# Kernel tuning notes

Measured on AMD Instinct MI355X. Metric: run time of the kernel, lower is better.

The kernel has to match this reference:

```python
import jax, jax.numpy as jnp
import numpy as np

EPS = 1e-7
LABEL_SMOOTHING = 0.1

def label2onehot(labels, pad_value):
    # labels: [B,T] int -> multi-hot [B, pad_value] with pad column dropped and index 0 zeroed
    oh = jax.nn.one_hot(labels, pad_value + 1, dtype=jnp.float32)  # [B,T,P+1]
    oh = oh.max(axis=1)[:, :-1]                                    # [B,P]
    return oh.at[:, 0].set(0.0)

def mask_from_eos(ids, eos_value):
    # mult_before=False variant: mask[:,0]=1, mask[:,t]=prod_{j=1..t}(ids[:,j]!=eos)
    ne = (ids != eos_value).astype(jnp.float32)
    ne = ne.at[:, 0].set(1.0)
    return jnp.cumprod(ne, axis=1)

def bce(p, t):
    p = jnp.clip(p, EPS, 1.0 - EPS)
    return -(t * jnp.log(p) + (1.0 - t) * jnp.log1p(-p))

def setup_inputs():
    key = jax.random.key(0)
    k1, k2, k3 = jax.random.split(key, 3)
    B, T, P = 4096, 20, 1488  # batch, max ingredients, ingredient vocab (= pad_value)
    return {
        "ingr_logits": jax.random.normal(k1, (B, T, P), dtype=jnp.float32),
        "target_ingrs": jax.random.randint(k2, (B, T), 0, P + 1, dtype=jnp.int32),
        "ingr_ids": jax.random.randint(k3, (B, T), 0, P + 1, dtype=jnp.int32),
        "pad_value": P,
    }

def reference(ingr_logits, target_ingrs, ingr_ids, pad_value):
    probs = jax.nn.softmax(ingr_logits, axis=-1)            # [B,T,P]
    eos = probs[:, :, 0]                                    # [B,T]

    t_oh = label2onehot(target_ingrs, pad_value)            # [B,P]
    denom = jnp.float32(t_oh.shape[-1])
    t_oh_smooth = jnp.where(t_oh == 0, LABEL_SMOOTHING / denom, 1.0 - LABEL_SMOOTHING)

    target_eos = ((target_ingrs == 0) ^ (target_ingrs == pad_value)).astype(jnp.float32)
    eos_pos = (target_ingrs == 0).astype(jnp.float32)
    eos_head = ((target_ingrs != pad_value) & (target_ingrs != 0)).astype(jnp.float32)

    mask = mask_from_eos(target_ingrs, 0)                   # [B,T]
    ingr_probs = (probs * mask[:, :, None]).max(axis=1)     # [B,P] permutation-invariant max
    ingr_ids_m = jnp.where(mask == 0, pad_value, ingr_ids)

    ingr_loss = bce(ingr_probs, t_oh_smooth).mean()

    card_penalty = (jnp.abs((ingr_probs * t_oh).sum(axis=1))
                    - t_oh.sum(axis=1)
                    + jnp.abs((ingr_probs * (1.0 - t_oh)).sum(axis=1)))

    eos_l = bce(eos, target_eos)                            # [B,T]
    mult = 0.5
    eos_loss = (mult * (eos_l * eos_pos).sum(axis=1) / (eos_pos.sum(axis=1) + 1e-6)
                + mult * (eos_l * eos_head).sum(axis=1) / (eos_head.sum(axis=1) + 1e-6))

    pred_oh = label2onehot(ingr_ids_m, pad_value)           # [B,P]
    num = (pred_oh * t_oh).sum(axis=1)
    den = (pred_oh + t_oh - pred_oh * t_oh).sum(axis=1) + 1e-6
    iou = 1.0 - num / den                                   # softIoU loss per sample

    return (ingr_loss, card_penalty, eos_loss, iou)
```

## Files before the change

kernel.cpp:

```cpp
#include <hip/hip_runtime.h>
#include <math.h>

#define BATCH 4096
#define TSEQ  20
#define PDIM  1488
#define PADV  1488
#define NV    372
#define NT    384
#define NW    6
#define EPSF  1e-7f

__device__ __forceinline__ float bce_f(float p, float t) {
    p = fminf(fmaxf(p, EPSF), 1.0f - EPSF);
    return -(t * logf(p) + (1.0f - t) * log1pf(-p));
}

__global__ __launch_bounds__(NT) void icm_main_kernel(
    const float* __restrict__ logits,
    const int*   __restrict__ target,
    const int*   __restrict__ ids,
    float*       __restrict__ out,
    float*       __restrict__ ws)
{
    const int b    = blockIdx.x;
    const int tid  = threadIdx.x;
    const int lane = tid & 63;
    const int wid  = tid >> 6;

    __shared__ int   s_tgt[TSEQ];
    __shared__ int   s_ids[TSEQ];
    __shared__ float s_mask[TSEQ];
    __shared__ float s_maxbuf[NW];
    __shared__ float s_sumbuf[NW];
    __shared__ unsigned char s_toh[PDIM];
    __shared__ unsigned char s_pred[PDIM];

    if (tid < NV) {
        ((int*)s_toh)[tid]  = 0;
        ((int*)s_pred)[tid] = 0;
    }
    if (tid < TSEQ) {
        s_tgt[tid] = target[b * TSEQ + tid];
        s_ids[tid] = ids[b * TSEQ + tid];
    }
    __syncthreads();

    if (tid == 0) {
        float m = 1.0f;
        s_mask[0] = 1.0f;
        for (int t = 1; t < TSEQ; ++t) {
            m *= (s_tgt[t] != 0) ? 1.0f : 0.0f;
            s_mask[t] = m;
        }
    }
    if (tid < TSEQ) {
        int v = s_tgt[tid];
        if (v >= 1 && v < PDIM) s_toh[v] = 1;
    }
    __syncthreads();
    if (tid < TSEQ) {
        int v = (s_mask[tid] != 0.0f) ? s_ids[tid] : PADV;
        if (v >= 1 && v < PDIM) s_pred[v] = 1;
    }

    const size_t row0 = (size_t)b * TSEQ * PDIM;

    float4 run = make_float4(0.f, 0.f, 0.f, 0.f);
    float acc_pos = 0.f, acc_head = 0.f, n_pos = 0.f, n_head = 0.f;

    float4 cur = make_float4(0.f, 0.f, 0.f, 0.f);
    if (tid < NV) cur = ((const float4*)(logits + row0))[tid];

    for (int t = 0; t < TSEQ; ++t) {
        float4 nxt = make_float4(0.f, 0.f, 0.f, 0.f);
        if (t + 1 < TSEQ && tid < NV)
            nxt = ((const float4*)(logits + row0 + (size_t)(t + 1) * PDIM))[tid];

        float vmax = -INFINITY;
        if (tid < NV) vmax = fmaxf(fmaxf(cur.x, cur.y), fmaxf(cur.z, cur.w));
        #pragma unroll
        for (int off = 32; off >= 1; off >>= 1)
            vmax = fmaxf(vmax, __shfl_down(vmax, off, 64));
        if (lane == 0) s_maxbuf[wid] = vmax;
        __syncthreads();
        float m = s_maxbuf[0];
        #pragma unroll
        for (int i = 1; i < NW; ++i) m = fmaxf(m, s_maxbuf[i]);

        float4 e = make_float4(0.f, 0.f, 0.f, 0.f);
        float vsum = 0.f;
        if (tid < NV) {
            e.x = __expf(cur.x - m);
            e.y = __expf(cur.y - m);
            e.z = __expf(cur.z - m);
            e.w = __expf(cur.w - m);
            vsum = (e.x + e.y) + (e.z + e.w);
        }
        #pragma unroll
        for (int off = 32; off >= 1; off >>= 1)
            vsum += __shfl_down(vsum, off, 64);
        if (lane == 0) s_sumbuf[wid] = vsum;
        __syncthreads();
        float s = s_sumbuf[0];
        #pragma unroll
        for (int i = 1; i < NW; ++i) s += s_sumbuf[i];
        float rinv = 1.0f / s;

        if (s_mask[t] != 0.0f && tid < NV) {
            run.x = fmaxf(run.x, e.x * rinv);
            run.y = fmaxf(run.y, e.y * rinv);
            run.z = fmaxf(run.z, e.z * rinv);
            run.w = fmaxf(run.w, e.w * rinv);
        }

        if (tid == 0) {
            float eosp = e.x * rinv;
            int   tv   = s_tgt[t];
            float te   = (tv == 0 || tv == PADV) ? 1.0f : 0.0f;
            float el   = bce_f(eosp, te);
            float ep   = (tv == 0) ? 1.0f : 0.0f;
            float eh   = (tv != 0 && tv != PADV) ? 1.0f : 0.0f;
            acc_pos  += el * ep;  n_pos  += ep;
            acc_head += el * eh;  n_head += eh;
        }

        cur = nxt;
    }

    __syncthreads();

    float bce_sum = 0.f, s1 = 0.f, s2 = 0.f, ntc = 0.f, inter = 0.f, uni = 0.f;
    if (tid < NV) {
        float rp[4] = {run.x, run.y, run.z, run.w};
        #pragma unroll
        for (int j = 0; j < 4; ++j) {
            int   p   = tid * 4 + j;
            float toh = (float)s_toh[p];
            float pr  = (float)s_pred[p];
            float ts  = (toh == 0.f) ? (0.1f / 1488.0f) : 0.9f;
            bce_sum += bce_f(rp[j], ts);
            s1      += rp[j] * toh;
            s2      += rp[j] * (1.f - toh);
            ntc     += toh;
            inter   += pr * toh;
            uni     += pr + toh - pr * toh;
        }
    }

    float vals[6] = {bce_sum, s1, s2, ntc, inter, uni};
    float tot[6];
    #pragma unroll
    for (int q = 0; q < 6; ++q) {
        float v = vals[q];
        #pragma unroll
        for (int off = 32; off >= 1; off >>= 1)
            v += __shfl_down(v, off, 64);
        if (lane == 0) s_sumbuf[wid] = v;
        __syncthreads();
        float r = s_sumbuf[0];
        #pragma unroll
        for (int i = 1; i < NW; ++i) r += s_sumbuf[i];
        tot[q] = r;
        __syncthreads();
    }

    if (tid == 0) {
        ws[b] = tot[0];
        out[1 + b] = fabsf(tot[1]) - tot[3] + fabsf(tot[2]);
        out[1 + BATCH + b] = 0.5f * acc_pos / (n_pos + 1e-6f)
                           + 0.5f * acc_head / (n_head + 1e-6f);
        out[1 + 2 * BATCH + b] = 1.0f - tot[4] / (tot[5] + 1e-6f);
    }
}

__global__ __launch_bounds__(256) void icm_reduce_kernel(
    const float* __restrict__ ws, float* __restrict__ out)
{
    int tid = threadIdx.x;
    float v = 0.f;
    for (int i = tid; i < BATCH; i += 256) v += ws[i];
    #pragma unroll
    for (int off = 32; off >= 1; off >>= 1) v += __shfl_down(v, off, 64);
    __shared__ float buf[4];
    int lane = tid & 63, wid = tid >> 6;
    if (lane == 0) buf[wid] = v;
    __syncthreads();
    if (tid == 0) {
        float t = (buf[0] + buf[1]) + (buf[2] + buf[3]);
        out[0] = t / ((float)BATCH * (float)PDIM);
    }
}

extern "C" void kernel_launch(void* const* d_in, const int* in_sizes, int n_in,
                              void* d_out, int out_size, void* d_ws, size_t ws_size,
                              hipStream_t stream) {
    const float* logits = (const float*)d_in[0];
    const int*   target = (const int*)d_in[1];
    const int*   ids    = (const int*)d_in[2];

    float* out = (float*)d_out;
    float* ws  = (float*)d_ws;

    hipLaunchKernelGGL(icm_main_kernel, dim3(BATCH), dim3(NT), 0, stream,
                       logits, target, ids, out, ws);
    hipLaunchKernelGGL(icm_reduce_kernel, dim3(1), dim3(256), 0, stream,
                       ws, out);
}
```

Baseline: 713.4 us.

## Map one batch row per wavefront with register bitmasks and double-buffered loads

Each batch row is now handled by a single 64-lane wavefront (four rows per 256-thread block) instead of a 384-thread block. All block-level __syncthreads and shared-memory reductions are replaced with wave shuffles. The one-hot and mask tables become per-lane bitmasks, and logits rows are loaded two timesteps ahead into alternating register buffers. This removes barrier and LDS overhead from the softmax per timestep and keeps more loads in flight, at the cost of higher register use per lane and a serial 20-step scan per wave.

```diff
diff --git a/kernel.cpp b/kernel.cpp
--- a/kernel.cpp
+++ b/kernel.cpp
@@ -5,9 +5,7 @@
 #define TSEQ  20
 #define PDIM  1488
 #define PADV  1488
-#define NV    372
-#define NT    384
-#define NW    6
+#define NSLOT 372
 #define EPSF  1e-7f
 
 __device__ __forceinline__ float bce_f(float p, float t) {
@@ -15,161 +13,202 @@
     return -(t * logf(p) + (1.0f - t) * log1pf(-p));
 }
 
-__global__ __launch_bounds__(NT) void icm_main_kernel(
+__device__ __forceinline__ float wave_max(float v) {
+    #pragma unroll
+    for (int m = 1; m < 64; m <<= 1) v = fmaxf(v, __shfl_xor(v, m, 64));
+    return v;
+}
+__device__ __forceinline__ float wave_sum(float v) {
+    #pragma unroll
+    for (int m = 1; m < 64; m <<= 1) v += __shfl_xor(v, m, 64);
+    return v;
+}
+
+__global__ __launch_bounds__(256) void icm_main_kernel(
     const float* __restrict__ logits,
     const int*   __restrict__ target,
     const int*   __restrict__ ids,
     float*       __restrict__ out,
     float*       __restrict__ ws)
 {
-    const int b    = blockIdx.x;
-    const int tid  = threadIdx.x;
-    const int lane = tid & 63;
-    const int wid  = tid >> 6;
-
-    __shared__ int   s_tgt[TSEQ];
-    __shared__ int   s_ids[TSEQ];
-    __shared__ float s_mask[TSEQ];
-    __shared__ float s_maxbuf[NW];
-    __shared__ float s_sumbuf[NW];
-    __shared__ unsigned char s_toh[PDIM];
-    __shared__ unsigned char s_pred[PDIM];
-
-    if (tid < NV) {
-        ((int*)s_toh)[tid]  = 0;
-        ((int*)s_pred)[tid] = 0;
-    }
-    if (tid < TSEQ) {
-        s_tgt[tid] = target[b * TSEQ + tid];
-        s_ids[tid] = ids[b * TSEQ + tid];
-    }
-    __syncthreads();
-
-    if (tid == 0) {
-        float m = 1.0f;
-        s_mask[0] = 1.0f;
-        for (int t = 1; t < TSEQ; ++t) {
-            m *= (s_tgt[t] != 0) ? 1.0f : 0.0f;
-            s_mask[t] = m;
-        }
-    }
-    if (tid < TSEQ) {
-        int v = s_tgt[tid];
-        if (v >= 1 && v < PDIM) s_toh[v] = 1;
-    }
-    __syncthreads();
-    if (tid < TSEQ) {
-        int v = (s_mask[tid] != 0.0f) ? s_ids[tid] : PADV;
-        if (v >= 1 && v < PDIM) s_pred[v] = 1;
-    }
-
-    const size_t row0 = (size_t)b * TSEQ * PDIM;
-
-    float4 run = make_float4(0.f, 0.f, 0.f, 0.f);
+    const int lane = threadIdx.x & 63;
+    const int wid  = threadIdx.x >> 6;
+    const int b    = blockIdx.x * 4 + wid;
+    if (b >= BATCH) return;
+
+    const bool v5 = (lane < 52);
+
+    int tvr = (lane < TSEQ) ? target[b * TSEQ + lane] : PADV;
+    int idr = (lane < TSEQ) ? ids[b * TSEQ + lane]    : PADV;
+
+    unsigned rowmask = 0, tohm = 0, predm = 0;
+    int ok = 1;
+    #pragma unroll
+    for (int j = 0; j < TSEQ; ++j) {
+        int v = __shfl(tvr, j, 64);
+        if (j > 0 && v == 0) ok = 0;
+        if (ok) rowmask |= 1u << j;
+        if (v >= 1 && v < PDIM) {
+            int s = v >> 2;
+            if ((s & 63) == lane) tohm |= 1u << (((s >> 6) << 2) | (v & 3));
+        }
+        int iv = __shfl(idr, j, 64);
+        int mv = ok ? iv : PADV;
+        if (mv >= 1 && mv < PDIM) {
+            int s = mv >> 2;
+            if ((s & 63) == lane) predm |= 1u << (((s >> 6) << 2) | (mv & 3));
+        }
+    }
+
+    const float4* base = (const float4*)(logits + (size_t)b * TSEQ * PDIM);
+    const int slot5 = v5 ? (lane + 320) : 371;
+
+    float4 run[6];
+    #pragma unroll
+    for (int k = 0; k < 6; ++k) run[k] = make_float4(0.f, 0.f, 0.f, 0.f);
+
     float acc_pos = 0.f, acc_head = 0.f, n_pos = 0.f, n_head = 0.f;
 
-    float4 cur = make_float4(0.f, 0.f, 0.f, 0.f);
-    if (tid < NV) cur = ((const float4*)(logits + row0))[tid];
-
-    for (int t = 0; t < TSEQ; ++t) {
-        float4 nxt = make_float4(0.f, 0.f, 0.f, 0.f);
-        if (t + 1 < TSEQ && tid < NV)
-            nxt = ((const float4*)(logits + row0 + (size_t)(t + 1) * PDIM))[tid];
-
-        float vmax = -INFINITY;
-        if (tid < NV) vmax = fmaxf(fmaxf(cur.x, cur.y), fmaxf(cur.z, cur.w));
-        #pragma unroll
-        for (int off = 32; off >= 1; off >>= 1)
-            vmax = fmaxf(vmax, __shfl_down(vmax, off, 64));
-        if (lane == 0) s_maxbuf[wid] = vmax;
-        __syncthreads();
-        float m = s_maxbuf[0];
-        #pragma unroll
-        for (int i = 1; i < NW; ++i) m = fmaxf(m, s_maxbuf[i]);
-
-        float4 e = make_float4(0.f, 0.f, 0.f, 0.f);
-        float vsum = 0.f;
-        if (tid < NV) {
-            e.x = __expf(cur.x - m);
-            e.y = __expf(cur.y - m);
-            e.z = __expf(cur.z - m);
-            e.w = __expf(cur.w - m);
-            vsum = (e.x + e.y) + (e.z + e.w);
-        }
-        #pragma unroll
-        for (int off = 32; off >= 1; off >>= 1)
-            vsum += __shfl_down(vsum, off, 64);
-        if (lane == 0) s_sumbuf[wid] = vsum;
-        __syncthreads();
-        float s = s_sumbuf[0];
-        #pragma unroll
-        for (int i = 1; i < NW; ++i) s += s_sumbuf[i];
-        float rinv = 1.0f / s;
-
-        if (s_mask[t] != 0.0f && tid < NV) {
-            run.x = fmaxf(run.x, e.x * rinv);
-            run.y = fmaxf(run.y, e.y * rinv);
-            run.z = fmaxf(run.z, e.z * rinv);
-            run.w = fmaxf(run.w, e.w * rinv);
-        }
-
-        if (tid == 0) {
-            float eosp = e.x * rinv;
-            int   tv   = s_tgt[t];
-            float te   = (tv == 0 || tv == PADV) ? 1.0f : 0.0f;
+    float4 A[6], B[6];
+
+    #pragma unroll
+    for (int k = 0; k < 5; ++k) A[k] = base[lane + 64 * k];
+    A[5] = base[slot5];
+
+    for (int t = 0; t < TSEQ; t += 2) {
+        {
+            const float4* p = base + (size_t)(t + 1) * NSLOT;
+            #pragma unroll
+            for (int k = 0; k < 5; ++k) B[k] = p[lane + 64 * k];
+            B[5] = p[slot5];
+        }
+
+        {
+            float vmax = -INFINITY;
+            #pragma unroll
+            for (int k = 0; k < 6; ++k) {
+                if (k < 5 || v5) {
+                    float4 v = A[k];
+                    vmax = fmaxf(vmax, fmaxf(fmaxf(v.x, v.y), fmaxf(v.z, v.w)));
+                }
+            }
+            vmax = wave_max(vmax);
+            float ssum = 0.f;
+            #pragma unroll
+            for (int k = 0; k < 6; ++k) {
+                bool val = (k < 5) || v5;
+                float4 v = A[k], e;
+                e.x = val ? __expf(v.x - vmax) : 0.f;
+                e.y = val ? __expf(v.y - vmax) : 0.f;
+                e.z = val ? __expf(v.z - vmax) : 0.f;
+                e.w = val ? __expf(v.w - vmax) : 0.f;
+                A[k] = e;
+                ssum += (e.x + e.y) + (e.z + e.w);
+            }
+            ssum = wave_sum(ssum);
+            float rinv = 1.0f / ssum;
+            if ((rowmask >> t) & 1) {
+                #pragma unroll
+                for (int k = 0; k < 6; ++k) {
+                    run[k].x = fmaxf(run[k].x, A[k].x * rinv);
+                    run[k].y = fmaxf(run[k].y, A[k].y * rinv);
+                    run[k].z = fmaxf(run[k].z, A[k].z * rinv);
+                    run[k].w = fmaxf(run[k].w, A[k].w * rinv);
+                }
+            }
+            float eosp = A[0].x * rinv;
+            int   tvt  = __shfl(tvr, t, 64);
+            float te   = (tvt == 0 || tvt == PADV) ? 1.f : 0.f;
             float el   = bce_f(eosp, te);
-            float ep   = (tv == 0) ? 1.0f : 0.0f;
-            float eh   = (tv != 0 && tv != PADV) ? 1.0f : 0.0f;
-            acc_pos  += el * ep;  n_pos  += ep;
-            acc_head += el * eh;  n_head += eh;
-        }
-
-        cur = nxt;
-    }
-
-    __syncthreads();
+            float ep   = (tvt == 0) ? 1.f : 0.f;
+            float eh   = (tvt != 0 && tvt != PADV) ? 1.f : 0.f;
+            acc_pos += el * ep;  n_pos += ep;
+            acc_head += el * eh; n_head += eh;
+        }
+
+        if (t + 2 < TSEQ) {
+            const float4* p = base + (size_t)(t + 2) * NSLOT;
+            #pragma unroll
+            for (int k = 0; k < 5; ++k) A[k] = p[lane + 64 * k];
+            A[5] = p[slot5];
+        }
+
+        {
+            float vmax = -INFINITY;
+            #pragma unroll
+            for (int k = 0; k < 6; ++k) {
+                if (k < 5 || v5) {
+                    float4 v = B[k];
+                    vmax = fmaxf(vmax, fmaxf(fmaxf(v.x, v.y), fmaxf(v.z, v.w)));
+                }
+            }
+            vmax = wave_max(vmax);
+            float ssum = 0.f;
+            #pragma unroll
+            for (int k = 0; k < 6; ++k) {
+                bool val = (k < 5) || v5;
+                float4 v = B[k], e;
+                e.x = val ? __expf(v.x - vmax) : 0.f;
+                e.y = val ? __expf(v.y - vmax) : 0.f;
+                e.z = val ? __expf(v.z - vmax) : 0.f;
+                e.w = val ? __expf(v.w - vmax) : 0.f;
+                B[k] = e;
+                ssum += (e.x + e.y) + (e.z + e.w);
+            }
+            ssum = wave_sum(ssum);
+            float rinv = 1.0f / ssum;
+            if ((rowmask >> (t + 1)) & 1) {
+                #pragma unroll
+                for (int k = 0; k < 6; ++k) {
+                    run[k].x = fmaxf(run[k].x, B[k].x * rinv);
+                    run[k].y = fmaxf(run[k].y, B[k].y * rinv);
+                    run[k].z = fmaxf(run[k].z, B[k].z * rinv);
+                    run[k].w = fmaxf(run[k].w, B[k].w * rinv);
+                }
+            }
+            float eosp = B[0].x * rinv;
+            int   tvt  = __shfl(tvr, t + 1, 64);
+            float te   = (tvt == 0 || tvt == PADV) ? 1.f : 0.f;
+            float el   = bce_f(eosp, te);
+            float ep   = (tvt == 0) ? 1.f : 0.f;
+            float eh   = (tvt != 0 && tvt != PADV) ? 1.f : 0.f;
+            acc_pos += el * ep;  n_pos += ep;
+            acc_head += el * eh; n_head += eh;
+        }
+    }
 
     float bce_sum = 0.f, s1 = 0.f, s2 = 0.f, ntc = 0.f, inter = 0.f, uni = 0.f;
-    if (tid < NV) {
-        float rp[4] = {run.x, run.y, run.z, run.w};
+    #pragma unroll
+    for (int k = 0; k < 6; ++k) {
+        if (k == 5 && !v5) break;
+        float rp[4] = {run[k].x, run[k].y, run[k].z, run[k].w};
         #pragma unroll
         for (int j = 0; j < 4; ++j) {
-            int   p   = tid * 4 + j;
-            float toh = (float)s_toh[p];
-            float pr  = (float)s_pred[p];
-            float ts  = (toh == 0.f) ? (0.1f / 1488.0f) : 0.9f;
+            float toh = ((tohm  >> (k * 4 + j)) & 1) ? 1.f : 0.f;
+            float pr  = ((predm >> (k * 4 + j)) & 1) ? 1.f : 0.f;
+            float ts  = (toh > 0.f) ? 0.9f : (0.1f / 1488.0f);
             bce_sum += bce_f(rp[j], ts);
-            s1      += rp[j] * toh;
-            s2      += rp[j] * (1.f - toh);
-            ntc     += toh;
-            inter   += pr * toh;
-            uni     += pr + toh - pr * toh;
-        }
-    }
-
-    float vals[6] = {bce_sum, s1, s2, ntc, inter, uni};
-    float tot[6];
-    #pragma unroll
-    for (int q = 0; q < 6; ++q) {
-        float v = vals[q];
-        #pragma unroll
-        for (int off = 32; off >= 1; off >>= 1)
-            v += __shfl_down(v, off, 64);
-        if (lane == 0) s_sumbuf[wid] = v;
-        __syncthreads();
-        float r = s_sumbuf[0];
-        #pragma unroll
-        for (int i = 1; i < NW; ++i) r += s_sumbuf[i];
-        tot[q] = r;
-        __syncthreads();
-    }
-
-    if (tid == 0) {
-        ws[b] = tot[0];
-        out[1 + b] = fabsf(tot[1]) - tot[3] + fabsf(tot[2]);
-        out[1 + BATCH + b] = 0.5f * acc_pos / (n_pos + 1e-6f)
-                           + 0.5f * acc_head / (n_head + 1e-6f);
-        out[1 + 2 * BATCH + b] = 1.0f - tot[4] / (tot[5] + 1e-6f);
+            s1    += rp[j] * toh;
+            s2    += rp[j] * (1.f - toh);
+            ntc   += toh;
+            inter += pr * toh;
+            uni   += pr + toh - pr * toh;
+        }
+    }
+
+    bce_sum = wave_sum(bce_sum);
+    s1      = wave_sum(s1);
+    s2      = wave_sum(s2);
+    ntc     = wave_sum(ntc);
+    inter   = wave_sum(inter);
+    uni     = wave_sum(uni);
+
+    if (lane == 0) {
+        ws[b] = bce_sum;
+        out[1 + b]             = fabsf(s1) - ntc + fabsf(s2);
+        out[1 + BATCH + b]     = 0.5f * acc_pos / (n_pos + 1e-6f)
+                               + 0.5f * acc_head / (n_head + 1e-6f);
+        out[1 + 2 * BATCH + b] = 1.0f - inter / (uni + 1e-6f);
     }
 }
 
@@ -180,7 +219,7 @@
     float v = 0.f;
     for (int i = tid; i < BATCH; i += 256) v += ws[i];
     #pragma unroll
-    for (int off = 32; off >= 1; off >>= 1) v += __shfl_down(v, off, 64);
+    for (int m = 1; m < 64; m <<= 1) v += __shfl_xor(v, m, 64);
     __shared__ float buf[4];
     int lane = tid & 63, wid = tid >> 6;
     if (lane == 0) buf[wid] = v;
@@ -201,7 +240,7 @@
     float* out = (float*)d_out;
     float* ws  = (float*)d_ws;
 
-    hipLaunchKernelGGL(icm_main_kernel, dim3(BATCH), dim3(NT), 0, stream,
+    hipLaunchKernelGGL(icm_main_kernel, dim3(BATCH / 4), dim3(256), 0, stream,
                        logits, target, ids, out, ws);
     hipLaunchKernelGGL(icm_reduce_kernel, dim3(1), dim3(256), 0, stream,
                        ws, out);
```

Result: faster. 659.0 us (-7.6%).
